# Kernel optimization log

Hardware: AMD Instinct MI355X
Metric: run time of the kernel (lower is better)

The kernel has to match this reference:

```python
import jax, jax.numpy as jnp
import numpy as np

EPS = 1e-5

def layernorm(x, gamma, beta):
    mu = jnp.mean(x, axis=-1, keepdims=True)
    var = jnp.var(x, axis=-1, keepdims=True)
    return (x - mu) * jax.lax.rsqrt(var + EPS) * gamma + beta

def setup_inputs() -> dict:
    key = jax.random.key(0)
    ks = jax.random.split(key, 8)
    B, N, D, H, Dh, M = 2, 2048, 768, 12, 64, 3072
    s = 0.02
    return {
        "x": jax.random.normal(ks[0], (B, N, D), jnp.float32),
        "Wqkv": jax.random.normal(ks[1], (D, 3 * H * Dh), jnp.float32) * s,
        "Wout": jax.random.normal(ks[2], (H * Dh, D), jnp.float32) * s,
        "gamma1": jnp.ones((D,), jnp.float32),
        "beta1": jnp.zeros((D,), jnp.float32),
        "gamma2": jnp.ones((D,), jnp.float32),
        "beta2": jnp.zeros((D,), jnp.float32),
        "W1": jax.random.normal(ks[3], (D, M), jnp.float32) * s,
        "b1": jnp.zeros((M,), jnp.float32),
        "W2": jax.random.normal(ks[4], (M, D), jnp.float32) * s,
        "b2": jnp.zeros((D,), jnp.float32),
        "attn_bias": jax.random.normal(ks[5], (1, H, N, N), jnp.float32) * 0.1,
    }

def reference(x, Wqkv, Wout, gamma1, beta1, gamma2, beta2, W1, b1, W2, b2, attn_bias):
    B, N, D = x.shape
    H = attn_bias.shape[1]
    Dh = Wqkv.shape[1] // (3 * H)
    scale = Dh ** -0.5
    # Attention block (pre-norm)
    h = layernorm(x, gamma1, beta1)
    qkv = h @ Wqkv                              # [B, N, 3*H*Dh]
    qkv = qkv.reshape(B, N, 3, H, Dh)
    q, k, v = (jnp.transpose(qkv[:, :, i], (0, 2, 1, 3)) for i in range(3))  # [B, H, N, Dh]
    dots = jnp.einsum('bhqd,bhkd->bhqk', q, k) * scale
    # pos_info == 'mul_att_normed'
    attn = jax.nn.softmax(dots, axis=-1) * jax.nn.softmax(attn_bias, axis=-1)
    attn = attn / jnp.sum(attn, axis=-1, keepdims=True)
    out = jnp.einsum('bhqk,bhkd->bhqd', attn, v)          # [B, H, N, Dh]
    out = jnp.transpose(out, (0, 2, 1, 3)).reshape(B, N, H * Dh)
    x = out @ Wout + x
    # FeedForward block (pre-norm)
    h = layernorm(x, gamma2, beta2)
    h = jax.nn.gelu(h @ W1 + b1, approximate=False)
    x = h @ W2 + b2 + x
    return x
```

## Files before the change

### kernel.cpp

```cpp
#include <hip/hip_runtime.h>

typedef unsigned short u16t;
typedef __bf16 bf16x8 __attribute__((ext_vector_type(8)));
typedef float  f32x4  __attribute__((ext_vector_type(4)));
typedef float  f32x16 __attribute__((ext_vector_type(16)));
typedef unsigned u32x2 __attribute__((ext_vector_type(2)));
typedef unsigned u32x4 __attribute__((ext_vector_type(4)));

#define DEV __device__ __forceinline__

DEV u16t f32_to_bf16(float f) {
    unsigned u = __float_as_uint(f);
    unsigned r = (u + 0x7FFFu + ((u >> 16) & 1u)) >> 16;
    return (u16t)r;
}
DEV float bf16_to_f32(u16t u) { return __uint_as_float((unsigned)u << 16); }

DEV unsigned cvt_pk_bf16(float lo, float hi) {
    unsigned r;
    asm("v_cvt_pk_bf16_f32 %0, %1, %2" : "=v"(r) : "v"(lo), "v"(hi));
    return r;
}

DEV float gelu_exact(float x) {
    return 0.5f * x * (1.0f + erff(x * 0.70710678118654752f));
}

DEV void glds16(const void* g, void* l) {
    __builtin_amdgcn_global_load_lds(
        (const __attribute__((address_space(1))) void*)g,
        (__attribute__((address_space(3))) void*)l, 16, 0, 0);
}

#define SCHED_FENCE() __builtin_amdgcn_sched_barrier(0)

#define WAITN_BARRIER(N)                                          \
    asm volatile("s_waitcnt vmcnt(" #N ")" ::: "memory");         \
    SCHED_FENCE();                                                \
    __builtin_amdgcn_s_barrier();                                 \
    SCHED_FENCE();

#define PLAIN_BARRIER()                                           \
    SCHED_FENCE();                                                \
    __builtin_amdgcn_s_barrier();                                 \
    SCHED_FENCE();

__global__ __launch_bounds__(256)
void ln_kernel(const float* __restrict__ x, const float* __restrict__ g,
               const float* __restrict__ b, u16t* __restrict__ out)
{
    const int row = blockIdx.x;
    const int t = threadIdx.x;
    const float* xr = x + (size_t)row * 768;
    float v0 = xr[t], v1 = xr[t + 256], v2 = xr[t + 512];
    float s = v0 + v1 + v2;
    float s2 = v0 * v0 + v1 * v1 + v2 * v2;
#pragma unroll
    for (int off = 32; off > 0; off >>= 1) {
        s  += __shfl_xor(s, off);
        s2 += __shfl_xor(s2, off);
    }
    __shared__ float sm[8];
    const int w = t >> 6;
    if ((t & 63) == 0) { sm[w] = s; sm[4 + w] = s2; }
    __syncthreads();
    s  = sm[0] + sm[1] + sm[2] + sm[3];
    s2 = sm[4] + sm[5] + sm[6] + sm[7];
    const float mu  = s * (1.0f / 768.0f);
    const float var = fmaxf(s2 * (1.0f / 768.0f) - mu * mu, 0.0f);
    const float rst = rsqrtf(var + 1e-5f);
    u16t* o = out + (size_t)row * 768;
    o[t]       = f32_to_bf16((v0 - mu) * rst * g[t]       + b[t]);
    o[t + 256] = f32_to_bf16((v1 - mu) * rst * g[t + 256] + b[t + 256]);
    o[t + 512] = f32_to_bf16((v2 - mu) * rst * g[t + 512] + b[t + 512]);
}

__global__ __launch_bounds__(256)
void transpose_cast(const float* __restrict__ in, u16t* __restrict__ out,
                    int R, int C)
{
    __shared__ float tile[64][65];
    const int c0 = blockIdx.x * 64, r0 = blockIdx.y * 64;
    const int t = threadIdx.x;
#pragma unroll
    for (int j = 0; j < 16; ++j) {
        const int idx = j * 256 + t;
        const int rl = idx >> 6, cl = idx & 63;
        tile[rl][cl] = in[(size_t)(r0 + rl) * C + c0 + cl];
    }
    __syncthreads();
#pragma unroll
    for (int j = 0; j < 16; ++j) {
        const int idx = j * 256 + t;
        const int cl = idx >> 6, rl = idx & 63;
        out[(size_t)(c0 + cl) * R + r0 + rl] = f32_to_bf16(tile[rl][cl]);
    }
}

template <int MODE>
__global__ __launch_bounds__(256)
void gemm_kernel(const u16t* __restrict__ A, const u16t* __restrict__ BT,
                 float* __restrict__ Cf, u16t* __restrict__ Cb,
                 const float* __restrict__ bias, const float* __restrict__ res,
                 u16t* __restrict__ Qo, u16t* __restrict__ Ko,
                 u16t* __restrict__ VTo,
                 int M, int Nn, int K)
{
    __shared__ __align__(16) char gsm[32768];
    const int t = threadIdx.x;
    const int w = t >> 6, lane = t & 63;
    const int l16 = lane & 15, lhi = lane >> 4;
    const int wr = w >> 1, wc = w & 1;
    const int m0 = blockIdx.x * 128, n0 = blockIdx.y * 128;

    const f32x4 fz = {0.f, 0.f, 0.f, 0.f};
    f32x4 acc[4][4];
#pragma unroll
    for (int i = 0; i < 4; ++i)
#pragma unroll
        for (int j = 0; j < 4; ++j) acc[i][j] = fz;

    const int srow = lane >> 2;
    const int sslot = ((lane & 3) ^ ((lane >> 3) & 3)) * 16;
    const int aswz = ((lhi ^ ((l16 >> 1) & 3)) << 4);

    auto stage = [&](int bufb, int kt) {
#pragma unroll
        for (int i = 0; i < 2; ++i) {
            const int row = w * 32 + i * 16 + srow;
            glds16((const char*)A + ((size_t)(m0 + row) * K + kt) * 2 + sslot,
                   gsm + bufb + w * 2048 + i * 1024);
            glds16((const char*)BT + ((size_t)(n0 + row) * K + kt) * 2 + sslot,
                   gsm + bufb + 8192 + w * 2048 + i * 1024);
        }
    };

    auto body = [&](int bufb) {
        const char* Ab = gsm + bufb;
        const char* Bb = gsm + bufb + 8192;
        bf16x8 af[4], bfv[4];
#pragma unroll
        for (int i = 0; i < 4; ++i)
            af[i] = *reinterpret_cast<const bf16x8*>(
                Ab + (64 * wr + 16 * i + l16) * 64 + aswz);
#pragma unroll
        for (int j = 0; j < 4; ++j)
            bfv[j] = *reinterpret_cast<const bf16x8*>(
                Bb + (64 * wc + 16 * j + l16) * 64 + aswz);
#pragma unroll
        for (int i = 0; i < 4; ++i)
#pragma unroll
            for (int j = 0; j < 4; ++j)
                acc[i][j] = __builtin_amdgcn_mfma_f32_16x16x32_bf16(
                    af[i], bfv[j], acc[i][j], 0, 0, 0);
    };

    stage(0, 0);
    int bufb = 0;
    for (int kt = 0; kt + 32 < K; kt += 32) {
        stage(bufb ^ 16384, kt + 32);
        WAITN_BARRIER(4)
        body(bufb);
        PLAIN_BARRIER()
        bufb ^= 16384;
    }
    WAITN_BARRIER(0)
    body(bufb);

    const int rb = m0 + 64 * wr + 4 * lhi;
    const int cb = n0 + 64 * wc + l16;

    if (MODE == 3) {
        const int qi = n0 / 768;
        const int b = rb >> 11;
        const int nn0 = rb & 2047;
#pragma unroll
        for (int j = 0; j < 4; ++j) {
            const int c = cb - qi * 768 + 16 * j;
            const int h = c >> 6, d = c & 63;
            if (qi < 2) {
                u16t* dst = (qi == 0) ? Qo : Ko;
                const size_t base = ((size_t)(b * 12 + h) * 2048 + nn0) * 64 + d;
#pragma unroll
                for (int i = 0; i < 4; ++i)
#pragma unroll
                    for (int r = 0; r < 4; ++r)
                        dst[base + (size_t)(16 * i + r) * 64] =
                            f32_to_bf16(acc[i][j][r]);
            } else {
                u16t* dst = VTo + ((size_t)(b * 12 + h) * 64 + d) * 2048 + nn0;
#pragma unroll
                for (int i = 0; i < 4; ++i) {
                    u32x2 pr;
                    pr[0] = cvt_pk_bf16(acc[i][j][0], acc[i][j][1]);
                    pr[1] = cvt_pk_bf16(acc[i][j][2], acc[i][j][3]);
                    *reinterpret_cast<u32x2*>(dst + 16 * i) = pr;
                }
            }
        }
        return;
    }

#pragma unroll
    for (int i = 0; i < 4; ++i) {
#pragma unroll
        for (int j = 0; j < 4; ++j) {
#pragma unroll
            for (int r = 0; r < 4; ++r) {
                const int row = rb + 16 * i + r;
                const int col = cb + 16 * j;
                float v = acc[i][j][r];
                if (MODE == 0) {
                    Cf[(size_t)row * Nn + col] = v;
                } else if (MODE == 1) {
                    v += res[(size_t)row * Nn + col];
                    if (bias) v += bias[col];
                    Cf[(size_t)row * Nn + col] = v;
                } else if (MODE == 2) {
                    v = gelu_exact(v + bias[col]);
                    Cb[(size_t)row * Nn + col] = f32_to_bf16(v);
                }
            }
        }
    }
}

__global__ __launch_bounds__(256, 2)
void attn_kernel(const u16t* __restrict__ Q, const u16t* __restrict__ K,
                 const u16t* __restrict__ VT, const float* __restrict__ bias,
                 u16t* __restrict__ Opart, float* __restrict__ Lpart)
{
    const int SEQ = 2048;
    const int h = blockIdx.y;
    const int ks = blockIdx.z;
    const int t = threadIdx.x;
    const int w = t >> 6, lane = t & 63;
    const int l32 = lane & 31, hi = lane >> 5;
    const int q = blockIdx.x * 128 + w * 32 + l32;
    const int bh0 = h, bh1 = 12 + h;

    __shared__ __align__(16) char smem[65536];

    const u16t* qp0 = Q + ((size_t)bh0 * SEQ + q) * 64 + 8 * hi;
    const u16t* qp1 = Q + ((size_t)bh1 * SEQ + q) * 64 + 8 * hi;
    bf16x8 qf0[4], qf1[4];
#pragma unroll
    for (int dseg = 0; dseg < 4; ++dseg) {
        qf0[dseg] = *reinterpret_cast<const bf16x8*>(qp0 + dseg * 16);
        qf1[dseg] = *reinterpret_cast<const bf16x8*>(qp1 + dseg * 16);
    }

    const char* kg0 = (const char*)K + (size_t)bh0 * SEQ * 128;
    const char* kg1 = (const char*)K + (size_t)bh1 * SEQ * 128;
    const char* vg0 = (const char*)VT + (size_t)bh0 * 64 * 4096;
    const char* vg1 = (const char*)VT + (size_t)bh1 * 64 * 4096;
    const char* bg = (const char*)bias +
                     ((size_t)h * SEQ + blockIdx.x * 128) * 8192;

    const int srow8 = lane >> 3;
    const int sslotK = ((lane & 7) ^ srow8) * 16;
    const int vrow  = w * 16 + (lane >> 2);
    const int sslotV = ((lane & 3) ^ ((vrow >> 1) & 3)) * 16;

    auto stage_all = [&](int bb, int k0) {
#pragma unroll
        for (int i = 0; i < 4; ++i) {
            const int row = 32 * w + 8 * i + srow8;
            glds16(bg + (size_t)row * 8192 + (size_t)k0 * 4 + sslotK,
                   smem + bb + 4096 * w + i * 1024);
        }
        glds16(kg0 + (size_t)(k0 + 8 * w + srow8) * 128 + sslotK,
               smem + bb + 16384 + w * 1024);
        glds16(kg1 + (size_t)(k0 + 8 * w + srow8) * 128 + sslotK,
               smem + bb + 20480 + w * 1024);
        glds16(vg0 + (size_t)vrow * 4096 + (size_t)k0 * 2 + sslotV,
               smem + bb + 24576 + w * 1024);
        glds16(vg1 + (size_t)vrow * 4096 + (size_t)k0 * 2 + sslotV,
               smem + bb + 28672 + w * 1024);
    };

    const int rsw = l32 & 7;
    int boff[4], koff[4];
#pragma unroll
    for (int g = 0; g < 4; ++g)
        boff[g] = (32 * w + l32) * 128 + ((((g << 1) + hi) ^ rsw) << 4);
#pragma unroll
    for (int dseg = 0; dseg < 4; ++dseg)
        koff[dseg] = l32 * 128 + ((((dseg << 1) + hi) ^ rsw) << 4);
    const int vr3 = (l32 >> 1) & 3;
    const int voff00 = l32 * 64 + ((hi ^ vr3) << 4);
    const int voff01 = l32 * 64 + (((2 + hi) ^ vr3) << 4);
    const int voff10 = voff00 + 32 * 64;
    const int voff11 = voff01 + 32 * 64;

    f32x16 o00, o01, o10, o11;
#pragma unroll
    for (int i = 0; i < 16; ++i) { o00[i] = 0.f; o01[i] = 0.f;
                                   o10[i] = 0.f; o11[i] = 0.f; }
    float lsum0 = 0.f, lsum1 = 0.f;

    auto batch_body = [&](const bf16x8 (&qf)[4], int kvbase, int vbase,
                          const f32x4 (&bv)[4], f32x16& oa, f32x16& ob,
                          float& lsum) {
        f32x16 st;
#pragma unroll
        for (int i = 0; i < 16; ++i) st[i] = 0.f;
#pragma unroll
        for (int dseg = 0; dseg < 4; ++dseg) {
            bf16x8 kf = *reinterpret_cast<const bf16x8*>(
                smem + kvbase + koff[dseg]);
            st = __builtin_amdgcn_mfma_f32_32x32x16_bf16(kf, qf[dseg], st, 0, 0, 0);
        }
        unsigned pk[8];
#pragma unroll
        for (int i2 = 0; i2 < 8; ++i2) {
            const int ia = 2 * i2, ib = 2 * i2 + 1;
            const float pa = __expf(st[ia] * 0.125f + bv[ia >> 2][ia & 3]);
            const float pb = __expf(st[ib] * 0.125f + bv[ib >> 2][ib & 3]);
            lsum += pa + pb;
            pk[i2] = cvt_pk_bf16(pa, pb);
        }
        unsigned sx[8];
#pragma unroll
        for (int i2 = 0; i2 < 8; ++i2)
            sx[i2] = (unsigned)__shfl_xor((int)pk[i2], 32);
        union { unsigned u[4]; bf16x8 v; } B0, B1;
        B0.u[0] = hi ? sx[2] : pk[0];
        B0.u[1] = hi ? sx[3] : pk[1];
        B0.u[2] = hi ? pk[2] : sx[0];
        B0.u[3] = hi ? pk[3] : sx[1];
        B1.u[0] = hi ? sx[6] : pk[4];
        B1.u[1] = hi ? sx[7] : pk[5];
        B1.u[2] = hi ? pk[6] : sx[4];
        B1.u[3] = hi ? pk[7] : sx[5];
        bf16x8 v00 = *reinterpret_cast<const bf16x8*>(smem + vbase + voff00);
        bf16x8 v01 = *reinterpret_cast<const bf16x8*>(smem + vbase + voff01);
        bf16x8 v10 = *reinterpret_cast<const bf16x8*>(smem + vbase + voff10);
        bf16x8 v11 = *reinterpret_cast<const bf16x8*>(smem + vbase + voff11);
        oa = __builtin_amdgcn_mfma_f32_32x32x16_bf16(v00, B0.v, oa, 0, 0, 0);
        oa = __builtin_amdgcn_mfma_f32_32x32x16_bf16(v01, B1.v, oa, 0, 0, 0);
        ob = __builtin_amdgcn_mfma_f32_32x32x16_bf16(v10, B0.v, ob, 0, 0, 0);
        ob = __builtin_amdgcn_mfma_f32_32x32x16_bf16(v11, B1.v, ob, 0, 0, 0);
    };

    const int kbeg = ks * 512;

    stage_all(0, kbeg);
    WAITN_BARRIER(0)

    int cur = 0;
    for (int i = 0; i < 16; ++i) {
        const int k0 = kbeg + 32 * i;
        if (i < 15) {
            stage_all(cur ^ 32768, k0 + 32);
            WAITN_BARRIER(8)
        } else {
            WAITN_BARRIER(0)
        }
        {
            f32x4 bv[4];
#pragma unroll
            for (int g = 0; g < 4; ++g)
                bv[g] = *reinterpret_cast<const f32x4*>(smem + cur + boff[g]);
            batch_body(qf0, cur + 16384, cur + 24576, bv, o00, o01, lsum0);
            batch_body(qf1, cur + 20480, cur + 28672, bv, o10, o11, lsum1);
        }
        PLAIN_BARRIER()
        cur ^= 32768;
    }

    lsum0 += __shfl_xor(lsum0, 32);
    lsum1 += __shfl_xor(lsum1, 32);

#pragma unroll
    for (int beta = 0; beta < 2; ++beta) {
        const int bh = beta ? bh1 : bh0;
        const f32x16& oa = beta ? o10 : o00;
        const f32x16& ob = beta ? o11 : o01;
        const float ls = beta ? lsum1 : lsum0;
        u16t* op = Opart + ((size_t)(ks * 24 + bh) * SEQ + q) * 64;
#pragma unroll
        for (int dh = 0; dh < 2; ++dh) {
            const f32x16& o = dh ? ob : oa;
#pragma unroll
            for (int g = 0; g < 4; ++g) {
                u32x2 pr;
                pr[0] = cvt_pk_bf16(o[4 * g], o[4 * g + 1]);
                pr[1] = cvt_pk_bf16(o[4 * g + 2], o[4 * g + 3]);
                *reinterpret_cast<u32x2*>(op + dh * 32 + 8 * g + 4 * hi) = pr;
            }
        }
        if (!hi)
            Lpart[(size_t)(ks * 24 + bh) * SEQ + q] = ls;
    }
}

__global__ __launch_bounds__(256)
void attn_combine(const u16t* __restrict__ Opart,
                  const float* __restrict__ Lpart, u16t* __restrict__ out)
{
    const int idx = blockIdx.x * 256 + threadIdx.x;
    const int dg = idx & 7;
    const int q = (idx >> 3) & 2047;
    const int bh = idx >> 14;
    const int b = bh / 12, h = bh % 12;
    const size_t base = ((size_t)bh * 2048 + q) * 64 + dg * 8;
    const size_t stride = (size_t)24 * 2048 * 64;
    float acc[8] = {0.f, 0.f, 0.f, 0.f, 0.f, 0.f, 0.f, 0.f};
    float l = 0.f;
#pragma unroll
    for (int j = 0; j < 4; ++j) {
        const u32x4 a = *reinterpret_cast<const u32x4*>(Opart + base + j * stride);
#pragma unroll
        for (int m = 0; m < 4; ++m) {
            acc[2 * m]     += bf16_to_f32((u16t)(a[m] & 0xFFFF));
            acc[2 * m + 1] += bf16_to_f32((u16t)(a[m] >> 16));
        }
        l += Lpart[(size_t)j * 24 * 2048 + bh * 2048 + q];
    }
    const float inv = 1.0f / l;
    u32x4 r;
#pragma unroll
    for (int m = 0; m < 4; ++m)
        r[m] = cvt_pk_bf16(acc[2 * m] * inv, acc[2 * m + 1] * inv);
    *reinterpret_cast<u32x4*>(
        out + ((size_t)(b * 2048 + q)) * 768 + h * 64 + dg * 8) = r;
}

extern "C" void kernel_launch(void* const* d_in, const int* in_sizes, int n_in,
                              void* d_out, int out_size, void* d_ws, size_t ws_size,
                              hipStream_t stream)
{
    const float* x    = (const float*)d_in[0];
    const float* Wqkv = (const float*)d_in[1];
    const float* Wout = (const float*)d_in[2];
    const float* g1   = (const float*)d_in[3];
    const float* be1  = (const float*)d_in[4];
    const float* g2   = (const float*)d_in[5];
    const float* be2  = (const float*)d_in[6];
    const float* W1   = (const float*)d_in[7];
    const float* b1   = (const float*)d_in[8];
    const float* W2   = (const float*)d_in[9];
    const float* b2   = (const float*)d_in[10];
    const float* ab   = (const float*)d_in[11];
    float* outp = (float*)d_out;

    char* ws = (char*)d_ws;
    size_t off = 0;
    auto alloc = [&](size_t bytes) -> char* {
        char* p = ws + off;
        off += (bytes + 255) & ~(size_t)255;
        return p;
    };

    u16t* WqkvT = (u16t*)alloc((size_t)2304 * 768 * 2);
    u16t* WoutT = (u16t*)alloc((size_t)768 * 768 * 2);
    u16t* W1T   = (u16t*)alloc((size_t)3072 * 768 * 2);
    u16t* W2T   = (u16t*)alloc((size_t)768 * 3072 * 2);
    u16t* h1    = (u16t*)alloc((size_t)4096 * 768 * 2);
    u16t* Qb    = (u16t*)alloc((size_t)24 * 2048 * 64 * 2);
    u16t* Kb    = (u16t*)alloc((size_t)24 * 2048 * 64 * 2);
    u16t* VTb   = (u16t*)alloc((size_t)24 * 64 * 2048 * 2);
    u16t* attnb = (u16t*)alloc((size_t)4096 * 768 * 2);
    float* x1   = (float*)alloc((size_t)4096 * 768 * 4);
    u16t* h2    = (u16t*)alloc((size_t)4096 * 768 * 2);
    u16t* Opart = (u16t*)alloc((size_t)4 * 24 * 2048 * 64 * 2);
    float* Lpart = (float*)alloc((size_t)4 * 24 * 2048 * 4);
    u16t* act   = (u16t*)alloc((size_t)4096 * 3072 * 2);

    transpose_cast<<<dim3(36, 12), 256, 0, stream>>>(Wqkv, WqkvT, 768, 2304);
    transpose_cast<<<dim3(12, 12), 256, 0, stream>>>(Wout, WoutT, 768, 768);
    transpose_cast<<<dim3(48, 12), 256, 0, stream>>>(W1,   W1T,   768, 3072);
    transpose_cast<<<dim3(12, 48), 256, 0, stream>>>(W2,   W2T,   3072, 768);

    ln_kernel<<<4096, 256, 0, stream>>>(x, g1, be1, h1);
    gemm_kernel<3><<<dim3(32, 18), 256, 0, stream>>>(
        h1, WqkvT, nullptr, nullptr, nullptr, nullptr, Qb, Kb, VTb,
        4096, 2304, 768);
    attn_kernel<<<dim3(16, 12, 4), 256, 0, stream>>>(Qb, Kb, VTb, ab, Opart, Lpart);
    attn_combine<<<(24 * 2048 * 8) / 256, 256, 0, stream>>>(Opart, Lpart, attnb);
    gemm_kernel<1><<<dim3(32, 6), 256, 0, stream>>>(
        attnb, WoutT, x1, nullptr, nullptr, x, nullptr, nullptr, nullptr,
        4096, 768, 768);

    ln_kernel<<<4096, 256, 0, stream>>>(x1, g2, be2, h2);
    gemm_kernel<2><<<dim3(32, 24), 256, 0, stream>>>(
        h2, W1T, nullptr, act, b1, nullptr, nullptr, nullptr, nullptr,
        4096, 3072, 768);
    gemm_kernel<1><<<dim3(32, 6), 256, 0, stream>>>(
        act, W2T, outp, nullptr, b2, x1, nullptr, nullptr, nullptr,
        4096, 768, 3072);
}
```

Measured before the change: 253.4 us.

## Double attention query tile per block, split keys 8 ways, merge weight transposes

Each attention block now covers 256 queries (two 128-query halves) and shares every staged K/V tile across both halves. The key range is split into 8 chunks instead of 4, so the grid stays at 768 blocks, and the combine kernel sums 8 partials. The aim is to halve K/V staging traffic per query. In exchange it uses 96KB of LDS, one block per CU, and twice as many live accumulators, and it doubles the partial-output buffer that the combine step has to read. The four weight transpose launches are also merged into a single kernel to cut launch overhead.

```diff
diff --git a/kernel.cpp b/kernel.cpp
--- a/kernel.cpp
+++ b/kernel.cpp
@@ -76,11 +76,19 @@
 }
 
 __global__ __launch_bounds__(256)
-void transpose_cast(const float* __restrict__ in, u16t* __restrict__ out,
-                    int R, int C)
+void transpose_all(const float* __restrict__ Wqkv, const float* __restrict__ Wout,
+                   const float* __restrict__ W1, const float* __restrict__ W2,
+                   u16t* __restrict__ WqkvT, u16t* __restrict__ WoutT,
+                   u16t* __restrict__ W1T, u16t* __restrict__ W2T)
 {
+    int b = blockIdx.x;
+    const float* in; u16t* out; int R, C, cx, ry;
+    if (b < 432)       { in = Wqkv; out = WqkvT; R = 768;  C = 2304; cx = b % 36; ry = b / 36; }
+    else if (b < 576)  { b -= 432;  in = Wout; out = WoutT; R = 768;  C = 768;  cx = b % 12; ry = b / 12; }
+    else if (b < 1152) { b -= 576;  in = W1;   out = W1T;   R = 768;  C = 3072; cx = b % 48; ry = b / 48; }
+    else               { b -= 1152; in = W2;   out = W2T;   R = 3072; C = 768;  cx = b % 12; ry = b / 12; }
     __shared__ float tile[64][65];
-    const int c0 = blockIdx.x * 64, r0 = blockIdx.y * 64;
+    const int c0 = cx * 64, r0 = ry * 64;
     const int t = threadIdx.x;
 #pragma unroll
     for (int j = 0; j < 16; ++j) {
@@ -225,7 +233,7 @@
     }
 }
 
-__global__ __launch_bounds__(256, 2)
+__global__ __launch_bounds__(256, 1)
 void attn_kernel(const u16t* __restrict__ Q, const u16t* __restrict__ K,
                  const u16t* __restrict__ VT, const float* __restrict__ bias,
                  u16t* __restrict__ Opart, float* __restrict__ Lpart)
@@ -236,26 +244,31 @@
     const int t = threadIdx.x;
     const int w = t >> 6, lane = t & 63;
     const int l32 = lane & 31, hi = lane >> 5;
-    const int q = blockIdx.x * 128 + w * 32 + l32;
+    const int q0 = blockIdx.x * 256;
+    const int qA = q0 + w * 32 + l32;
+    const int qB = qA + 128;
     const int bh0 = h, bh1 = 12 + h;
 
-    __shared__ __align__(16) char smem[65536];
-
-    const u16t* qp0 = Q + ((size_t)bh0 * SEQ + q) * 64 + 8 * hi;
-    const u16t* qp1 = Q + ((size_t)bh1 * SEQ + q) * 64 + 8 * hi;
-    bf16x8 qf0[4], qf1[4];
+    __shared__ __align__(16) char smem[98304];
+
+    const u16t* qpA0 = Q + ((size_t)bh0 * SEQ + qA) * 64 + 8 * hi;
+    const u16t* qpA1 = Q + ((size_t)bh1 * SEQ + qA) * 64 + 8 * hi;
+    const u16t* qpB0 = Q + ((size_t)bh0 * SEQ + qB) * 64 + 8 * hi;
+    const u16t* qpB1 = Q + ((size_t)bh1 * SEQ + qB) * 64 + 8 * hi;
+    bf16x8 qfA0[4], qfA1[4], qfB0[4], qfB1[4];
 #pragma unroll
     for (int dseg = 0; dseg < 4; ++dseg) {
-        qf0[dseg] = *reinterpret_cast<const bf16x8*>(qp0 + dseg * 16);
-        qf1[dseg] = *reinterpret_cast<const bf16x8*>(qp1 + dseg * 16);
+        qfA0[dseg] = *reinterpret_cast<const bf16x8*>(qpA0 + dseg * 16);
+        qfA1[dseg] = *reinterpret_cast<const bf16x8*>(qpA1 + dseg * 16);
+        qfB0[dseg] = *reinterpret_cast<const bf16x8*>(qpB0 + dseg * 16);
+        qfB1[dseg] = *reinterpret_cast<const bf16x8*>(qpB1 + dseg * 16);
     }
 
     const char* kg0 = (const char*)K + (size_t)bh0 * SEQ * 128;
     const char* kg1 = (const char*)K + (size_t)bh1 * SEQ * 128;
     const char* vg0 = (const char*)VT + (size_t)bh0 * 64 * 4096;
     const char* vg1 = (const char*)VT + (size_t)bh1 * 64 * 4096;
-    const char* bg = (const char*)bias +
-                     ((size_t)h * SEQ + blockIdx.x * 128) * 8192;
+    const char* bg = (const char*)bias + ((size_t)h * SEQ + q0) * 8192;
 
     const int srow8 = lane >> 3;
     const int sslotK = ((lane & 7) ^ srow8) * 16;
@@ -264,26 +277,29 @@
 
     auto stage_all = [&](int bb, int k0) {
 #pragma unroll
-        for (int i = 0; i < 4; ++i) {
-            const int row = 32 * w + 8 * i + srow8;
+        for (int i = 0; i < 8; ++i) {
+            const int row = 64 * w + 8 * i + srow8;
             glds16(bg + (size_t)row * 8192 + (size_t)k0 * 4 + sslotK,
-                   smem + bb + 4096 * w + i * 1024);
+                   smem + bb + 8192 * w + i * 1024);
         }
         glds16(kg0 + (size_t)(k0 + 8 * w + srow8) * 128 + sslotK,
-               smem + bb + 16384 + w * 1024);
+               smem + bb + 32768 + w * 1024);
         glds16(kg1 + (size_t)(k0 + 8 * w + srow8) * 128 + sslotK,
-               smem + bb + 20480 + w * 1024);
+               smem + bb + 36864 + w * 1024);
         glds16(vg0 + (size_t)vrow * 4096 + (size_t)k0 * 2 + sslotV,
-               smem + bb + 24576 + w * 1024);
+               smem + bb + 40960 + w * 1024);
         glds16(vg1 + (size_t)vrow * 4096 + (size_t)k0 * 2 + sslotV,
-               smem + bb + 28672 + w * 1024);
+               smem + bb + 45056 + w * 1024);
     };
 
     const int rsw = l32 & 7;
-    int boff[4], koff[4];
-#pragma unroll
-    for (int g = 0; g < 4; ++g)
-        boff[g] = (32 * w + l32) * 128 + ((((g << 1) + hi) ^ rsw) << 4);
+    int boffA[4], boffB[4], koff[4];
+#pragma unroll
+    for (int g = 0; g < 4; ++g) {
+        const int sz = (((g << 1) + hi) ^ rsw) << 4;
+        boffA[g] = (32 * w + l32) * 128 + sz;
+        boffB[g] = boffA[g] + 128 * 128;
+    }
 #pragma unroll
     for (int dseg = 0; dseg < 4; ++dseg)
         koff[dseg] = l32 * 128 + ((((dseg << 1) + hi) ^ rsw) << 4);
@@ -293,11 +309,13 @@
     const int voff10 = voff00 + 32 * 64;
     const int voff11 = voff01 + 32 * 64;
 
-    f32x16 o00, o01, o10, o11;
-#pragma unroll
-    for (int i = 0; i < 16; ++i) { o00[i] = 0.f; o01[i] = 0.f;
-                                   o10[i] = 0.f; o11[i] = 0.f; }
-    float lsum0 = 0.f, lsum1 = 0.f;
+    f32x16 oA00, oA01, oA10, oA11, oB00, oB01, oB10, oB11;
+#pragma unroll
+    for (int i = 0; i < 16; ++i) {
+        oA00[i] = 0.f; oA01[i] = 0.f; oA10[i] = 0.f; oA11[i] = 0.f;
+        oB00[i] = 0.f; oB01[i] = 0.f; oB10[i] = 0.f; oB11[i] = 0.f;
+    }
+    float lsA0 = 0.f, lsA1 = 0.f, lsB0 = 0.f, lsB1 = 0.f;
 
     auto batch_body = [&](const bf16x8 (&qf)[4], int kvbase, int vbase,
                           const f32x4 (&bv)[4], f32x16& oa, f32x16& ob,
@@ -343,17 +361,17 @@
         ob = __builtin_amdgcn_mfma_f32_32x32x16_bf16(v11, B1.v, ob, 0, 0, 0);
     };
 
-    const int kbeg = ks * 512;
+    const int kbeg = ks * 256;
 
     stage_all(0, kbeg);
     WAITN_BARRIER(0)
 
     int cur = 0;
-    for (int i = 0; i < 16; ++i) {
+    for (int i = 0; i < 8; ++i) {
         const int k0 = kbeg + 32 * i;
-        if (i < 15) {
-            stage_all(cur ^ 32768, k0 + 32);
-            WAITN_BARRIER(8)
+        if (i < 7) {
+            stage_all(cur ^ 49152, k0 + 32);
+            WAITN_BARRIER(12)
         } else {
             WAITN_BARRIER(0)
         }
@@ -361,38 +379,48 @@
             f32x4 bv[4];
 #pragma unroll
             for (int g = 0; g < 4; ++g)
-                bv[g] = *reinterpret_cast<const f32x4*>(smem + cur + boff[g]);
-            batch_body(qf0, cur + 16384, cur + 24576, bv, o00, o01, lsum0);
-            batch_body(qf1, cur + 20480, cur + 28672, bv, o10, o11, lsum1);
+                bv[g] = *reinterpret_cast<const f32x4*>(smem + cur + boffA[g]);
+            batch_body(qfA0, cur + 32768, cur + 40960, bv, oA00, oA01, lsA0);
+            batch_body(qfA1, cur + 36864, cur + 45056, bv, oA10, oA11, lsA1);
+#pragma unroll
+            for (int g = 0; g < 4; ++g)
+                bv[g] = *reinterpret_cast<const f32x4*>(smem + cur + boffB[g]);
+            batch_body(qfB0, cur + 32768, cur + 40960, bv, oB00, oB01, lsB0);
+            batch_body(qfB1, cur + 36864, cur + 45056, bv, oB10, oB11, lsB1);
         }
         PLAIN_BARRIER()
-        cur ^= 32768;
-    }
-
-    lsum0 += __shfl_xor(lsum0, 32);
-    lsum1 += __shfl_xor(lsum1, 32);
-
-#pragma unroll
-    for (int beta = 0; beta < 2; ++beta) {
-        const int bh = beta ? bh1 : bh0;
-        const f32x16& oa = beta ? o10 : o00;
-        const f32x16& ob = beta ? o11 : o01;
-        const float ls = beta ? lsum1 : lsum0;
-        u16t* op = Opart + ((size_t)(ks * 24 + bh) * SEQ + q) * 64;
-#pragma unroll
-        for (int dh = 0; dh < 2; ++dh) {
-            const f32x16& o = dh ? ob : oa;
-#pragma unroll
-            for (int g = 0; g < 4; ++g) {
-                u32x2 pr;
-                pr[0] = cvt_pk_bf16(o[4 * g], o[4 * g + 1]);
-                pr[1] = cvt_pk_bf16(o[4 * g + 2], o[4 * g + 3]);
-                *reinterpret_cast<u32x2*>(op + dh * 32 + 8 * g + 4 * hi) = pr;
-            }
+        cur ^= 49152;
+    }
+
+    lsA0 += __shfl_xor(lsA0, 32);
+    lsA1 += __shfl_xor(lsA1, 32);
+    lsB0 += __shfl_xor(lsB0, 32);
+    lsB1 += __shfl_xor(lsB1, 32);
+
+    auto store_out = [&](const f32x16& oa, const f32x16& ob, float ls,
+                         int bh, int qq) {
+        u16t* op = Opart + ((size_t)(ks * 24 + bh) * SEQ + qq) * 64;
+#pragma unroll
+        for (int g = 0; g < 4; ++g) {
+            u32x2 pr;
+            pr[0] = cvt_pk_bf16(oa[4 * g], oa[4 * g + 1]);
+            pr[1] = cvt_pk_bf16(oa[4 * g + 2], oa[4 * g + 3]);
+            *reinterpret_cast<u32x2*>(op + 8 * g + 4 * hi) = pr;
+        }
+#pragma unroll
+        for (int g = 0; g < 4; ++g) {
+            u32x2 pr;
+            pr[0] = cvt_pk_bf16(ob[4 * g], ob[4 * g + 1]);
+            pr[1] = cvt_pk_bf16(ob[4 * g + 2], ob[4 * g + 3]);
+            *reinterpret_cast<u32x2*>(op + 32 + 8 * g + 4 * hi) = pr;
         }
         if (!hi)
-            Lpart[(size_t)(ks * 24 + bh) * SEQ + q] = ls;
-    }
+            Lpart[(size_t)(ks * 24 + bh) * SEQ + qq] = ls;
+    };
+    store_out(oA00, oA01, lsA0, bh0, qA);
+    store_out(oA10, oA11, lsA1, bh1, qA);
+    store_out(oB00, oB01, lsB0, bh0, qB);
+    store_out(oB10, oB11, lsB1, bh1, qB);
 }
 
 __global__ __launch_bounds__(256)
@@ -409,7 +437,7 @@
     float acc[8] = {0.f, 0.f, 0.f, 0.f, 0.f, 0.f, 0.f, 0.f};
     float l = 0.f;
 #pragma unroll
-    for (int j = 0; j < 4; ++j) {
+    for (int j = 0; j < 8; ++j) {
         const u32x4 a = *reinterpret_cast<const u32x4*>(Opart + base + j * stride);
 #pragma unroll
         for (int m = 0; m < 4; ++m) {
@@ -464,20 +492,18 @@
     u16t* attnb = (u16t*)alloc((size_t)4096 * 768 * 2);
     float* x1   = (float*)alloc((size_t)4096 * 768 * 4);
     u16t* h2    = (u16t*)alloc((size_t)4096 * 768 * 2);
-    u16t* Opart = (u16t*)alloc((size_t)4 * 24 * 2048 * 64 * 2);
-    float* Lpart = (float*)alloc((size_t)4 * 24 * 2048 * 4);
+    u16t* Opart = (u16t*)alloc((size_t)8 * 24 * 2048 * 64 * 2);
+    float* Lpart = (float*)alloc((size_t)8 * 24 * 2048 * 4);
     u16t* act   = (u16t*)alloc((size_t)4096 * 3072 * 2);
 
-    transpose_cast<<<dim3(36, 12), 256, 0, stream>>>(Wqkv, WqkvT, 768, 2304);
-    transpose_cast<<<dim3(12, 12), 256, 0, stream>>>(Wout, WoutT, 768, 768);
-    transpose_cast<<<dim3(48, 12), 256, 0, stream>>>(W1,   W1T,   768, 3072);
-    transpose_cast<<<dim3(12, 48), 256, 0, stream>>>(W2,   W2T,   3072, 768);
+    transpose_all<<<1728, 256, 0, stream>>>(Wqkv, Wout, W1, W2,
+                                            WqkvT, WoutT, W1T, W2T);
 
     ln_kernel<<<4096, 256, 0, stream>>>(x, g1, be1, h1);
     gemm_kernel<3><<<dim3(32, 18), 256, 0, stream>>>(
         h1, WqkvT, nullptr, nullptr, nullptr, nullptr, Qb, Kb, VTb,
         4096, 2304, 768);
-    attn_kernel<<<dim3(16, 12, 4), 256, 0, stream>>>(Qb, Kb, VTb, ab, Opart, Lpart);
+    attn_kernel<<<dim3(8, 12, 8), 256, 0, stream>>>(Qb, Kb, VTb, ab, Opart, Lpart);
     attn_combine<<<(24 * 2048 * 8) / 256, 256, 0, stream>>>(Opart, Lpart, attnb);
     gemm_kernel<1><<<dim3(32, 6), 256, 0, stream>>>(
         attnb, WoutT, x1, nullptr, nullptr, x, nullptr, nullptr, nullptr,
```

Measured after the change: 275.6 us. 8.7% more time.
